# Optimization experiments

Measured on AMD Instinct MI355X. Metric: run time of the kernel, lower is better.

The kernel has to match this reference:

```python
import jax, jax.numpy as jnp
import numpy as np

H = 12          # num heads
D = 768         # hidden size
DH = D // H     # size per head
FF = 3072       # intermediate size
EPS = 1e-11


def gelu(x):
    # tanh approximation, matching the TF source exactly
    c = np.sqrt(2.0 / np.pi).astype(np.float32)
    return x * 0.5 * (1.0 + jnp.tanh(c * (x + 0.044715 * jnp.power(x, 3))))


def layer_norm(x, gamma, beta):
    mean = jnp.mean(x, axis=-1, keepdims=True)
    var = jnp.mean(jnp.square(x - mean), axis=-1, keepdims=True)
    return (x - mean) * jax.lax.rsqrt(var + EPS) * gamma + beta


def setup_inputs() -> dict:
    key = jax.random.key(0)
    ks = jax.random.split(key, 12)
    B, S = 16, 512
    std = 0.02
    inp = {
        "x": jax.random.normal(ks[0], (B, S, D), jnp.float32),
        "mask": jnp.ones((B, S), dtype=bool),
        "Wq": jax.random.normal(ks[1], (D, D), jnp.float32) * std,
        "bq": jnp.zeros((D,), jnp.float32),
        "Wk": jax.random.normal(ks[2], (D, D), jnp.float32) * std,
        "bk": jnp.zeros((D,), jnp.float32),
        "Wv": jax.random.normal(ks[3], (D, D), jnp.float32) * std,
        "bv": jnp.zeros((D,), jnp.float32),
        "Wo": jax.random.normal(ks[4], (D, D), jnp.float32) * std,
        "bo": jnp.zeros((D,), jnp.float32),
        "g1": jnp.ones((D,), jnp.float32),
        "b1": jnp.zeros((D,), jnp.float32),
        "Wi": jax.random.normal(ks[5], (D, FF), jnp.float32) * std,
        "bi": jnp.zeros((FF,), jnp.float32),
        "Wo2": jax.random.normal(ks[6], (FF, D), jnp.float32) * std,
        "bo2": jnp.zeros((D,), jnp.float32),
        "g2": jnp.ones((D,), jnp.float32),
        "b2": jnp.zeros((D,), jnp.float32),
    }
    return inp


def reference(x, mask, Wq, bq, Wk, bk, Wv, bv, Wo, bo, g1, b1, Wi, bi, Wo2, bo2, g2, b2):
    B, S, _ = x.shape
    # QKV projections
    q = (x @ Wq + bq).reshape(B, S, H, DH)
    k = (x @ Wk + bk).reshape(B, S, H, DH)
    v = (x @ Wv + bv).reshape(B, S, H, DH)
    # scaled dot-product attention scores [B, H, S, S]
    scores = jnp.einsum("bqhd,bkhd->bhqk", q, k) / np.sqrt(DH).astype(np.float32)
    # key-side mask, applied as score * m + (1 - m) * -100 (per original source)
    m = mask[:, None, None, :].astype(jnp.float32)
    scores = scores * m + (1.0 - m) * (-100.0)
    probs = jax.nn.softmax(scores, axis=-1)
    attn = jnp.einsum("bhqk,bkhd->bqhd", probs, v).reshape(B, S, D)
    # tf.boolean_mask with all-True mask -> flatten batch and seq dims
    attn = attn.reshape(B * S, D)
    x_flat = x.reshape(B * S, D)
    # attention output projection + residual + LN
    attn_out = layer_norm(attn @ Wo + bo + x_flat, g1, b1)
    # FFN: gelu dense then output dense + residual + LN
    inter = gelu(attn_out @ Wi + bi)
    out = layer_norm(inter @ Wo2 + bo2 + attn_out, g2, b2)
    return out
```

## Files before the change

kernel.cpp:

```cpp
#include <hip/hip_runtime.h>


#define DEV __device__ __forceinline__

typedef unsigned short u16;
typedef unsigned int   u32;
typedef __bf16 bf16x8 __attribute__((ext_vector_type(8)));
typedef float  f32x4  __attribute__((ext_vector_type(4)));
typedef unsigned short u16x8 __attribute__((ext_vector_type(8)));
typedef unsigned short u16x4 __attribute__((ext_vector_type(4)));

DEV u16 f2bf(float f) {
    u32 u = __builtin_bit_cast(u32, f);
    u += 0x7fffu + ((u >> 16) & 1u);
    return (u16)(u >> 16);
}

DEV float gelu_f(float x) {
    float u = 0.7978845608028654f * (x + 0.044715f * x * x * x);
    float e = __expf(2.f * u);
    return 0.5f * x * (2.f - 2.f / (e + 1.f));
}

DEV void gload16(const void* gsrc, void* ldst) {
    __builtin_amdgcn_global_load_lds(
        (__attribute__((address_space(1))) void*)(void*)(const_cast<void*>(gsrc)),
        (__attribute__((address_space(3))) void*)ldst, 16, 0, 0);
}

DEV f32x4 MFMA(bf16x8 a, bf16x8 b, f32x4 c) {
    return __builtin_amdgcn_mfma_f32_16x16x32_bf16(a, b, c, 0, 0, 0);
}

__global__ __launch_bounds__(256) void cvt_bf16(const float* __restrict__ in,
                                                u16* __restrict__ out, int n) {
    int i = (blockIdx.x * 256 + threadIdx.x) * 4;
    if (i >= n) return;
    f32x4 v = *(const f32x4*)(in + i);
    u16x4 o;
    o.x = f2bf(v.x); o.y = f2bf(v.y); o.z = f2bf(v.z); o.w = f2bf(v.w);
    *(u16x4*)(out + i) = o;
}

__global__ __launch_bounds__(256) void transpose_cvt(const float* __restrict__ in,
                                                     u16* __restrict__ out,
                                                     int R, int C) {
    __shared__ float tile[32][33];
    int tx = threadIdx.x & 31, ty = threadIdx.x >> 5;
    int r0 = blockIdx.y * 32, c0 = blockIdx.x * 32;
#pragma unroll
    for (int i = 0; i < 4; i++)
        tile[ty + i * 8][tx] = in[(size_t)(r0 + ty + i * 8) * C + c0 + tx];
    __syncthreads();
#pragma unroll
    for (int i = 0; i < 4; i++)
        out[(size_t)(c0 + ty + i * 8) * R + r0 + tx] = f2bf(tile[tx][ty + i * 8]);
}

__global__ void concat_bias(const float* __restrict__ bq, const float* __restrict__ bk,
                            const float* __restrict__ bv, float* __restrict__ o) {
    int i = blockIdx.x * 256 + threadIdx.x;
    if (i < 2304) o[i] = (i < 768) ? bq[i] : (i < 1536 ? bk[i - 768] : bv[i - 1536]);
}

template <int EPI>
DEV void gemm_hi_body(const u16* __restrict__ A, const u16* __restrict__ BT,
                      const float* __restrict__ bias, void* __restrict__ Cout,
                      int N, int K, int ntn) {
    __shared__ __align__(16) char smem[32768];
    const int t = threadIdx.x, lane = t & 63, wid = t >> 6;
    const int nwg = gridDim.x, bid = blockIdx.x;
    const int swzb = ((nwg & 7) == 0) ? ((bid & 7) * (nwg >> 3) + (bid >> 3)) : bid;
    const int tm = swzb / ntn, tn = swzb % ntn;
    const int wm = wid >> 1, wn = wid & 1;

    f32x4 acc[4][4];
#pragma unroll
    for (int i = 0; i < 4; i++)
#pragma unroll
        for (int j = 0; j < 4; j++) acc[i][j] = f32x4{0.f, 0.f, 0.f, 0.f};

    const int NT = K >> 5;
    const u16* Ab = A + (size_t)tm * 128 * K;
    const u16* Bb = BT + (size_t)tn * 128 * K;

    int sr[2], sc[2];
#pragma unroll
    for (int j = 0; j < 2; j++) {
        int X = t * 16 + j * 4096;
        int Y = X ^ (((X >> 7) & 7) << 4);
        sr[j] = Y >> 6;
        sc[j] = (Y & 63) >> 1;
    }
    const u16* pA0 = Ab + (size_t)sr[0] * K + sc[0];
    const u16* pA1 = Ab + (size_t)sr[1] * K + sc[1];
    const u16* pB0 = Bb + (size_t)sr[0] * K + sc[0];
    const u16* pB1 = Bb + (size_t)sr[1] * K + sc[1];
    const int d0 = wid * 1024, d1 = wid * 1024 + 4096;

    const int g16 = (lane >> 4) << 4;
    const int rA = wm * 64 + (lane & 15);
    const int rB = wn * 64 + (lane & 15);
    const int aoff = (rA * 64 + g16) ^ (((rA >> 1) & 7) << 4);
    const int boff = 8192 + ((rB * 64 + g16) ^ (((rB >> 1) & 7) << 4));

#define STG(KT, BUF)                                                  \
    {                                                                 \
        char* s_ = smem + (BUF) * 16384;                              \
        gload16(pA0 + (KT), s_ + d0);                                 \
        gload16(pA1 + (KT), s_ + d1);                                 \
        gload16(pB0 + (KT), s_ + 8192 + d0);                          \
        gload16(pB1 + (KT), s_ + 8192 + d1);                          \
    }

    STG(0, 0);
    __syncthreads();

    for (int kt = 0; kt < NT; ++kt) {
        if (kt + 1 < NT) STG((kt + 1) << 5, (kt & 1) ^ 1);
        const char* buf = smem + (kt & 1) * 16384;
        bf16x8 af[4], bfr[4];
#pragma unroll
        for (int mi = 0; mi < 4; mi++) af[mi] = *(const bf16x8*)(buf + aoff + mi * 1024);
#pragma unroll
        for (int ni = 0; ni < 4; ni++) bfr[ni] = *(const bf16x8*)(buf + boff + ni * 1024);
        __builtin_amdgcn_s_setprio(1);
#pragma unroll
        for (int mi = 0; mi < 4; mi++)
#pragma unroll
            for (int ni = 0; ni < 4; ni++)
                acc[mi][ni] = MFMA(af[mi], bfr[ni], acc[mi][ni]);
        __builtin_amdgcn_s_setprio(0);
        __syncthreads();
    }
#undef STG

    const int r0 = tm * 128 + wm * 64, c0 = tn * 128 + wn * 64;
    float bcol[4];
#pragma unroll
    for (int ni = 0; ni < 4; ni++) bcol[ni] = bias[c0 + ni * 16 + (lane & 15)];
#pragma unroll
    for (int mi = 0; mi < 4; mi++) {
#pragma unroll
        for (int r = 0; r < 4; r++) {
            int gr = r0 + mi * 16 + ((lane >> 4) << 2) + r;
#pragma unroll
            for (int ni = 0; ni < 4; ni++) {
                int gc = c0 + ni * 16 + (lane & 15);
                float v = acc[mi][ni][r] + bcol[ni];
                if constexpr (EPI == 2) v = gelu_f(v);
                if constexpr (EPI == 1)
                    ((float*)Cout)[(size_t)gr * N + gc] = v;
                else
                    ((u16*)Cout)[(size_t)gr * N + gc] = f2bf(v);
            }
        }
    }
}

__global__ __launch_bounds__(256, 4) void gemm_qkv(const u16* __restrict__ A,
                                                   const u16* __restrict__ BT,
                                                   const float* __restrict__ bias,
                                                   void* __restrict__ Cout,
                                                   int N, int K, int ntn) {
    gemm_hi_body<0>(A, BT, bias, Cout, N, K, ntn);
}
__global__ __launch_bounds__(256, 4) void gemm_wo(const u16* __restrict__ A,
                                                  const u16* __restrict__ BT,
                                                  const float* __restrict__ bias,
                                                  void* __restrict__ Cout,
                                                  int N, int K, int ntn) {
    gemm_hi_body<1>(A, BT, bias, Cout, N, K, ntn);
}
__global__ __launch_bounds__(256, 4) void gemm_ffn1(const u16* __restrict__ A,
                                                    const u16* __restrict__ BT,
                                                    const float* __restrict__ bias,
                                                    void* __restrict__ Cout,
                                                    int N, int K, int ntn) {
    gemm_hi_body<2>(A, BT, bias, Cout, N, K, ntn);
}
__global__ __launch_bounds__(256, 4) void gemm_ffn2(const u16* __restrict__ A,
                                                    const u16* __restrict__ BT,
                                                    const float* __restrict__ bias,
                                                    void* __restrict__ Cout,
                                                    int N, int K, int ntn) {
    gemm_hi_body<1>(A, BT, bias, Cout, N, K, ntn);
}

__global__ __launch_bounds__(256) void attn_kernel(const u16* __restrict__ QKV,
                                                   u16* __restrict__ attnb) {
    __shared__ __align__(16) char sm[24576];
    char* Ks = sm;
    char* Vt = sm + 8192;
    const int t = threadIdx.x, lane = t & 63, wid = t >> 6;
    const int qt = blockIdx.x, bh = blockIdx.y;
    const int b = bh / 12, h = bh % 12;
    const size_t base = (size_t)b * 512 * 2304;
    char* Pw = sm + 16384 + wid * 2048;

    bf16x8 aq[2];
    {
        int qrow = qt * 64 + wid * 16 + (lane & 15);
        const u16* qp = QKV + base + (size_t)qrow * 2304 + h * 64 + ((lane >> 4) << 3);
        aq[0] = *(const bf16x8*)qp;
        aq[1] = *(const bf16x8*)(qp + 32);
    }
    f32x4 oacc[4];
#pragma unroll
    for (int g = 0; g < 4; g++) oacc[g] = f32x4{0.f, 0.f, 0.f, 0.f};
    float mrun[4] = {-1e30f, -1e30f, -1e30f, -1e30f};
    float lrun[4] = {0.f, 0.f, 0.f, 0.f};

    for (int kt = 0; kt < 8; ++kt) {
        __syncthreads();
#pragma unroll
        for (int i = 0; i < 2; i++) {
            int cw = wid * 2 + i;
            int o = cw * 1024 + lane * 16;
            int row = o >> 7;
            int cb = (o & 127) ^ ((row & 7) << 4);
            gload16(QKV + base + (size_t)(kt * 64 + row) * 2304 + 768 + h * 64 + (cb >> 1),
                    Ks + cw * 1024);
        }
        {
            int key = t & 63, dh0 = wid * 16;
            const u16* vp = QKV + base + (size_t)(kt * 64 + key) * 2304 + 1536 + h * 64 + dh0;
            u16x8 v0 = *(const u16x8*)vp;
            u16x8 v1 = *(const u16x8*)(vp + 8);
#pragma unroll
            for (int j = 0; j < 8; j++) {
                int dh = dh0 + j;
                *(u16*)(Vt + dh * 128 + ((key * 2) ^ ((dh & 7) << 4))) = v0[j];
            }
#pragma unroll
            for (int j = 0; j < 8; j++) {
                int dh = dh0 + 8 + j;
                *(u16*)(Vt + dh * 128 + ((key * 2) ^ ((dh & 7) << 4))) = v1[j];
            }
        }
        __syncthreads();

        f32x4 sacc[4];
#pragma unroll
        for (int ni = 0; ni < 4; ni++) sacc[ni] = f32x4{0.f, 0.f, 0.f, 0.f};
#pragma unroll
        for (int ni = 0; ni < 4; ni++) {
            int row = ni * 16 + (lane & 15);
#pragma unroll
            for (int ks = 0; ks < 2; ks++) {
                int cb = (ks * 64 + ((lane >> 4) << 4)) ^ ((row & 7) << 4);
                bf16x8 bk = *(const bf16x8*)(Ks + row * 128 + cb);
                sacc[ni] = MFMA(aq[ks], bk, sacc[ni]);
            }
        }
#pragma unroll
        for (int ni = 0; ni < 4; ni++)
#pragma unroll
            for (int r = 0; r < 4; r++) sacc[ni][r] *= 0.125f;

#pragma unroll
        for (int r = 0; r < 4; r++) {
            float pm = fmaxf(fmaxf(sacc[0][r], sacc[1][r]), fmaxf(sacc[2][r], sacc[3][r]));
            pm = fmaxf(pm, __shfl_xor(pm, 1));
            pm = fmaxf(pm, __shfl_xor(pm, 2));
            pm = fmaxf(pm, __shfl_xor(pm, 4));
            pm = fmaxf(pm, __shfl_xor(pm, 8));
            float mnew = fmaxf(mrun[r], pm);
            float sf = __expf(mrun[r] - mnew);
            mrun[r] = mnew;
            lrun[r] *= sf;
#pragma unroll
            for (int g = 0; g < 4; g++) oacc[g][r] *= sf;
            int prow = ((lane >> 4) << 2) + r;
            float ps = 0.f;
#pragma unroll
            for (int ni = 0; ni < 4; ni++) {
                float p = __expf(sacc[ni][r] - mnew);
                ps += p;
                int col = ni * 16 + (lane & 15);
                *(u16*)(Pw + prow * 128 + ((col * 2) ^ ((prow & 7) << 4))) = f2bf(p);
            }
            ps += __shfl_xor(ps, 1);
            ps += __shfl_xor(ps, 2);
            ps += __shfl_xor(ps, 4);
            ps += __shfl_xor(ps, 8);
            lrun[r] += ps;
        }
        __syncthreads();

#pragma unroll
        for (int ks = 0; ks < 2; ks++) {
            int prow = lane & 15;
            int pcb = (ks * 64 + ((lane >> 4) << 4)) ^ ((prow & 7) << 4);
            bf16x8 ap = *(const bf16x8*)(Pw + prow * 128 + pcb);
#pragma unroll
            for (int g = 0; g < 4; g++) {
                int vrow = g * 16 + (lane & 15);
                int vcb = (ks * 64 + ((lane >> 4) << 4)) ^ ((vrow & 7) << 4);
                bf16x8 bv = *(const bf16x8*)(Vt + vrow * 128 + vcb);
                oacc[g] = MFMA(ap, bv, oacc[g]);
            }
        }
    }

#pragma unroll
    for (int g = 0; g < 4; g++)
#pragma unroll
        for (int r = 0; r < 4; r++) {
            int qrow = qt * 64 + wid * 16 + ((lane >> 4) << 2) + r;
            float o = oacc[g][r] / lrun[r];
            attnb[(size_t)(b * 512 + qrow) * 768 + h * 64 + g * 16 + (lane & 15)] = f2bf(o);
        }
}

__global__ __launch_bounds__(256) void ln_kernel(const float* __restrict__ Y,
                                                 const float* __restrict__ res,
                                                 const float* __restrict__ g,
                                                 const float* __restrict__ bta,
                                                 float* __restrict__ outf,
                                                 u16* __restrict__ outb) {
    int row = blockIdx.x, t = threadIdx.x, lane = t & 63, wid = t >> 6;
    const float* y = Y + (size_t)row * 768;
    const float* rr = res + (size_t)row * 768;
    float v[3];
#pragma unroll
    for (int i = 0; i < 3; i++) v[i] = y[t + i * 256] + rr[t + i * 256];

    float s = v[0] + v[1] + v[2];
#pragma unroll
    for (int o = 32; o; o >>= 1) s += __shfl_xor(s, o);
    __shared__ float sm[4];
    __shared__ float bc[2];
    if (lane == 0) sm[wid] = s;
    __syncthreads();
    if (t == 0) bc[0] = (sm[0] + sm[1] + sm[2] + sm[3]) * (1.f / 768.f);
    __syncthreads();
    float mean = bc[0];

    float q = 0.f;
#pragma unroll
    for (int i = 0; i < 3; i++) { float d = v[i] - mean; q += d * d; }
#pragma unroll
    for (int o = 32; o; o >>= 1) q += __shfl_xor(q, o);
    if (lane == 0) sm[wid] = q;
    __syncthreads();
    if (t == 0) bc[1] = rsqrtf((sm[0] + sm[1] + sm[2] + sm[3]) * (1.f / 768.f) + 1e-11f);
    __syncthreads();
    float rs = bc[1];
#pragma unroll
    for (int i = 0; i < 3; i++) {
        int c = t + i * 256;
        float o = (v[i] - mean) * rs * g[c] + bta[c];
        outf[(size_t)row * 768 + c] = o;
        if (outb) outb[(size_t)row * 768 + c] = f2bf(o);
    }
}

extern "C" void kernel_launch(void* const* d_in, const int* in_sizes, int n_in,
                              void* d_out, int out_size, void* d_ws, size_t ws_size,
                              hipStream_t stream) {
    const float* x   = (const float*)d_in[0];
    const float* Wq  = (const float*)d_in[2];
    const float* bq  = (const float*)d_in[3];
    const float* Wk  = (const float*)d_in[4];
    const float* bk  = (const float*)d_in[5];
    const float* Wv  = (const float*)d_in[6];
    const float* bv  = (const float*)d_in[7];
    const float* Wo  = (const float*)d_in[8];
    const float* bo  = (const float*)d_in[9];
    const float* g1  = (const float*)d_in[10];
    const float* b1  = (const float*)d_in[11];
    const float* Wi  = (const float*)d_in[12];
    const float* bi  = (const float*)d_in[13];
    const float* Wo2 = (const float*)d_in[14];
    const float* bo2 = (const float*)d_in[15];
    const float* g2  = (const float*)d_in[16];
    const float* b2  = (const float*)d_in[17];

    char* w = (char*)d_ws;
    size_t off = 0;
    auto alloc = [&](size_t n) { size_t o = off; off += (n + 255) & ~(size_t)255; return o; };
    size_t oXb    = alloc((size_t)8192 * 768 * 2);
    size_t oWqkvT = alloc((size_t)2304 * 768 * 2);
    size_t oWoT   = alloc((size_t)768 * 768 * 2);
    size_t oWiT   = alloc((size_t)3072 * 768 * 2);
    size_t oWo2T  = alloc((size_t)768 * 3072 * 2);
    size_t oBqkv  = alloc((size_t)2304 * 4);
    size_t oR0    = alloc((size_t)8192 * 3072 * 2);
    size_t oY     = alloc((size_t)8192 * 768 * 4);
    size_t oAof   = alloc((size_t)8192 * 768 * 4);
    size_t oAob   = alloc((size_t)8192 * 768 * 2);
    (void)ws_size; (void)in_sizes; (void)n_in; (void)out_size;

    u16*   Xb    = (u16*)(w + oXb);
    u16*   WqkvT = (u16*)(w + oWqkvT);
    u16*   WoT   = (u16*)(w + oWoT);
    u16*   WiT   = (u16*)(w + oWiT);
    u16*   Wo2T  = (u16*)(w + oWo2T);
    float* bqkv  = (float*)(w + oBqkv);
    u16*   QKV   = (u16*)(w + oR0);
    u16*   attnb = (u16*)(w + oR0 + (size_t)8192 * 2304 * 2);
    u16*   inter = (u16*)(w + oR0);
    float* Y     = (float*)(w + oY);
    float* aof   = (float*)(w + oAof);
    u16*   aob   = (u16*)(w + oAob);

    cvt_bf16<<<6144, 256, 0, stream>>>(x, Xb, 8192 * 768);
    transpose_cvt<<<dim3(24, 24), 256, 0, stream>>>(Wq, WqkvT, 768, 768);
    transpose_cvt<<<dim3(24, 24), 256, 0, stream>>>(Wk, WqkvT + 768 * 768, 768, 768);
    transpose_cvt<<<dim3(24, 24), 256, 0, stream>>>(Wv, WqkvT + 2 * 768 * 768, 768, 768);
    transpose_cvt<<<dim3(24, 24), 256, 0, stream>>>(Wo, WoT, 768, 768);
    transpose_cvt<<<dim3(96, 24), 256, 0, stream>>>(Wi, WiT, 768, 3072);
    transpose_cvt<<<dim3(24, 96), 256, 0, stream>>>(Wo2, Wo2T, 3072, 768);
    concat_bias<<<9, 256, 0, stream>>>(bq, bk, bv, bqkv);

    gemm_qkv<<<1152, 256, 0, stream>>>(Xb, WqkvT, bqkv, QKV, 2304, 768, 18);
    attn_kernel<<<dim3(8, 192), 256, 0, stream>>>(QKV, attnb);
    gemm_wo<<<384, 256, 0, stream>>>(attnb, WoT, bo, Y, 768, 768, 6);
    ln_kernel<<<8192, 256, 0, stream>>>(Y, x, g1, b1, aof, aob);
    gemm_ffn1<<<1536, 256, 0, stream>>>(aob, WiT, bi, inter, 3072, 768, 24);
    gemm_ffn2<<<384, 256, 0, stream>>>(inter, Wo2T, bo2, Y, 768, 3072, 6);
    ln_kernel<<<8192, 256, 0, stream>>>(Y, aof, g2, b2, (float*)d_out, nullptr);
}
```

Measured before the change: 281.1 us.

## Use 256x256-tile 8-wave pipelined GEMM for QKV and FFN1 projections

Adds a new GEMM kernel with 512 threads and a 256x256 output tile. It double-buffers 128 KB of LDS and interleaves the next chunk's global loads with MFMA phases, using barriers and s_setprio. The QKV and FFN1 projections move to this kernel, with fewer, larger workgroups, to raise data reuse per tile and overlap loads with compute. In exchange, LDS and register use rise sharply, limiting occupancy. The QKV grid of 288 blocks may also underfill the CUs or leave tail imbalance.

```diff
diff --git a/kernel.cpp b/kernel.cpp
--- a/kernel.cpp
+++ b/kernel.cpp
@@ -61,6 +61,169 @@
                             const float* __restrict__ bv, float* __restrict__ o) {
     int i = blockIdx.x * 256 + threadIdx.x;
     if (i < 2304) o[i] = (i < 768) ? bq[i] : (i < 1536 ? bk[i - 768] : bv[i - 1536]);
+}
+
+template <int EPI>
+DEV void gemm8p_body(const u16* __restrict__ A, const u16* __restrict__ BT,
+                     const float* __restrict__ bias, void* __restrict__ Cout,
+                     int N, int K, int ntn) {
+    __shared__ __align__(16) char smem[131072];
+    const int t = threadIdx.x, lane = t & 63, wid = t >> 6;
+    const int nwg = gridDim.x, bid = blockIdx.x;
+    const int swzb = ((nwg & 7) == 0) ? ((bid & 7) * (nwg >> 3) + (bid >> 3)) : bid;
+    const int tm = swzb / ntn, tn = swzb % ntn;
+    const int wm = wid >> 2, wn = wid & 3;
+
+    f32x4 acc[8][4];
+#pragma unroll
+    for (int m = 0; m < 8; m++)
+#pragma unroll
+        for (int n = 0; n < 4; n++) acc[m][n] = f32x4{0.f, 0.f, 0.f, 0.f};
+
+    const int NC = K >> 6;
+    const u16* Abp = A + (size_t)tm * 256 * K;
+    const u16* Bbp = BT + (size_t)tn * 256 * K;
+
+    int sr[2], sc[2];
+#pragma unroll
+    for (int j = 0; j < 2; j++) {
+        int X = t * 16 + j * 8192;
+        int Y = X ^ (((X >> 7) & 7) << 4);
+        sr[j] = Y >> 7;
+        sc[j] = (Y & 127) >> 1;
+    }
+    const u16* pA0 = Abp + (size_t)sr[0] * K + sc[0];
+    const u16* pA1 = Abp + (size_t)sr[1] * K + sc[1];
+    const u16* pB0 = Bbp + (size_t)sr[0] * K + sc[0];
+    const u16* pB1 = Bbp + (size_t)sr[1] * K + sc[1];
+    const int dst0 = wid * 1024, dst1 = wid * 1024 + 8192;
+
+    const int l15 = lane & 15, g16 = (lane >> 4) << 4, sw = (lane & 7) << 4;
+    const int aHB = wm * 16384;
+    const int bHB = 32768 + (wn >> 1) * 16384 + (wn & 1) * 8192;
+    const int rb = l15 * 128;
+    const int cb0 = g16 ^ sw, cb1 = (64 + g16) ^ sw;
+
+#define STG_A(C, H) { char* d_ = smem + ((C) & 1) * 65536 + (H) * 16384;      \
+    gload16(pA0 + (size_t)(H) * 128 * K + (size_t)(C) * 64, d_ + dst0);       \
+    gload16(pA1 + (size_t)(H) * 128 * K + (size_t)(C) * 64, d_ + dst1); }
+#define STG_B(C, H) { char* d_ = smem + ((C) & 1) * 65536 + 32768 + (H) * 16384; \
+    gload16(pB0 + (size_t)(H) * 128 * K + (size_t)(C) * 64, d_ + dst0);       \
+    gload16(pB1 + (size_t)(H) * 128 * K + (size_t)(C) * 64, d_ + dst1); }
+#define BAR  __builtin_amdgcn_s_barrier(); asm volatile("" ::: "memory");
+
+    STG_A(0, 0) STG_A(0, 1) STG_B(0, 0) STG_B(0, 1) STG_A(1, 0) STG_A(1, 1)
+    asm volatile("s_waitcnt vmcnt(4)" ::: "memory");
+    BAR
+
+    for (int c = 0; c < NC; ++c) {
+        const char* db = smem + (c & 1) * 65536;
+        bf16x8 Alo[4][2], Ahi[4][2], Bf[4][2];
+#pragma unroll
+        for (int mi = 0; mi < 4; mi++) {
+            Alo[mi][0] = *(const bf16x8*)(db + aHB + rb + mi * 2048 + cb0);
+            Alo[mi][1] = *(const bf16x8*)(db + aHB + rb + mi * 2048 + cb1);
+        }
+#pragma unroll
+        for (int ni = 0; ni < 4; ni++) {
+            Bf[ni][0] = *(const bf16x8*)(db + bHB + rb + ni * 2048 + cb0);
+            Bf[ni][1] = *(const bf16x8*)(db + bHB + rb + ni * 2048 + cb1);
+        }
+        if (c + 1 < NC) STG_B(c + 1, 0)
+        BAR
+        asm volatile("s_waitcnt lgkmcnt(0)" ::: "memory");
+        __builtin_amdgcn_s_setprio(1);
+#pragma unroll
+        for (int mi = 0; mi < 4; mi++)
+#pragma unroll
+            for (int ni = 0; ni < 2; ni++)
+#pragma unroll
+                for (int ks = 0; ks < 2; ks++)
+                    acc[mi][ni] = MFMA(Alo[mi][ks], Bf[ni][ks], acc[mi][ni]);
+        __builtin_amdgcn_s_setprio(0);
+        BAR
+#pragma unroll
+        for (int mi = 0; mi < 4; mi++) {
+            Ahi[mi][0] = *(const bf16x8*)(db + aHB + 8192 + rb + mi * 2048 + cb0);
+            Ahi[mi][1] = *(const bf16x8*)(db + aHB + 8192 + rb + mi * 2048 + cb1);
+        }
+        if (c + 1 < NC) STG_B(c + 1, 1)
+        BAR
+        asm volatile("s_waitcnt lgkmcnt(0)" ::: "memory");
+        __builtin_amdgcn_s_setprio(1);
+#pragma unroll
+        for (int mi = 0; mi < 4; mi++)
+#pragma unroll
+            for (int ni = 2; ni < 4; ni++)
+#pragma unroll
+                for (int ks = 0; ks < 2; ks++)
+                    acc[mi][ni] = MFMA(Alo[mi][ks], Bf[ni][ks], acc[mi][ni]);
+        __builtin_amdgcn_s_setprio(0);
+        BAR
+        if (c + 2 < NC) STG_A(c + 2, 0)
+        BAR
+        __builtin_amdgcn_s_setprio(1);
+#pragma unroll
+        for (int mi = 0; mi < 4; mi++)
+#pragma unroll
+            for (int ni = 0; ni < 2; ni++)
+#pragma unroll
+                for (int ks = 0; ks < 2; ks++)
+                    acc[4 + mi][ni] = MFMA(Ahi[mi][ks], Bf[ni][ks], acc[4 + mi][ni]);
+        __builtin_amdgcn_s_setprio(0);
+        BAR
+        if (c + 2 < NC) STG_A(c + 2, 1)
+        BAR
+        __builtin_amdgcn_s_setprio(1);
+#pragma unroll
+        for (int mi = 0; mi < 4; mi++)
+#pragma unroll
+            for (int ni = 2; ni < 4; ni++)
+#pragma unroll
+                for (int ks = 0; ks < 2; ks++)
+                    acc[4 + mi][ni] = MFMA(Ahi[mi][ks], Bf[ni][ks], acc[4 + mi][ni]);
+        __builtin_amdgcn_s_setprio(0);
+        if (c + 2 < NC) asm volatile("s_waitcnt vmcnt(4)" ::: "memory");
+        else            asm volatile("s_waitcnt vmcnt(0)" ::: "memory");
+        BAR
+    }
+#undef STG_A
+#undef STG_B
+#undef BAR
+
+    const int r0 = tm * 256 + wm * 128, c0 = tn * 256 + wn * 64;
+    float cb4[4];
+#pragma unroll
+    for (int ni = 0; ni < 4; ni++) cb4[ni] = bias[c0 + ni * 16 + l15];
+#pragma unroll
+    for (int m = 0; m < 8; m++) {
+#pragma unroll
+        for (int r = 0; r < 4; r++) {
+            int gr = r0 + m * 16 + ((lane >> 4) << 2) + r;
+#pragma unroll
+            for (int ni = 0; ni < 4; ni++) {
+                int gc = c0 + ni * 16 + l15;
+                float v = acc[m][ni][r] + cb4[ni];
+                if constexpr (EPI == 2) v = gelu_f(v);
+                ((u16*)Cout)[(size_t)gr * N + gc] = f2bf(v);
+            }
+        }
+    }
+}
+
+__global__ __launch_bounds__(512, 2) void g8_qkv(const u16* __restrict__ A,
+                                                 const u16* __restrict__ BT,
+                                                 const float* __restrict__ bias,
+                                                 void* __restrict__ Cout,
+                                                 int N, int K, int ntn) {
+    gemm8p_body<0>(A, BT, bias, Cout, N, K, ntn);
+}
+__global__ __launch_bounds__(512, 2) void g8_ffn1(const u16* __restrict__ A,
+                                                  const u16* __restrict__ BT,
+                                                  const float* __restrict__ bias,
+                                                  void* __restrict__ Cout,
+                                                  int N, int K, int ntn) {
+    gemm8p_body<2>(A, BT, bias, Cout, N, K, ntn);
 }
 
 template <int EPI>
@@ -158,26 +321,12 @@
     }
 }
 
-__global__ __launch_bounds__(256, 4) void gemm_qkv(const u16* __restrict__ A,
-                                                   const u16* __restrict__ BT,
-                                                   const float* __restrict__ bias,
-                                                   void* __restrict__ Cout,
-                                                   int N, int K, int ntn) {
-    gemm_hi_body<0>(A, BT, bias, Cout, N, K, ntn);
-}
 __global__ __launch_bounds__(256, 4) void gemm_wo(const u16* __restrict__ A,
                                                   const u16* __restrict__ BT,
                                                   const float* __restrict__ bias,
                                                   void* __restrict__ Cout,
                                                   int N, int K, int ntn) {
     gemm_hi_body<1>(A, BT, bias, Cout, N, K, ntn);
-}
-__global__ __launch_bounds__(256, 4) void gemm_ffn1(const u16* __restrict__ A,
-                                                    const u16* __restrict__ BT,
-                                                    const float* __restrict__ bias,
-                                                    void* __restrict__ Cout,
-                                                    int N, int K, int ntn) {
-    gemm_hi_body<2>(A, BT, bias, Cout, N, K, ntn);
 }
 __global__ __launch_bounds__(256, 4) void gemm_ffn2(const u16* __restrict__ A,
                                                     const u16* __restrict__ BT,
@@ -414,11 +563,11 @@
     transpose_cvt<<<dim3(24, 96), 256, 0, stream>>>(Wo2, Wo2T, 3072, 768);
     concat_bias<<<9, 256, 0, stream>>>(bq, bk, bv, bqkv);
 
-    gemm_qkv<<<1152, 256, 0, stream>>>(Xb, WqkvT, bqkv, QKV, 2304, 768, 18);
+    g8_qkv<<<288, 512, 0, stream>>>(Xb, WqkvT, bqkv, QKV, 2304, 768, 9);
     attn_kernel<<<dim3(8, 192), 256, 0, stream>>>(QKV, attnb);
     gemm_wo<<<384, 256, 0, stream>>>(attnb, WoT, bo, Y, 768, 768, 6);
     ln_kernel<<<8192, 256, 0, stream>>>(Y, x, g1, b1, aof, aob);
-    gemm_ffn1<<<1536, 256, 0, stream>>>(aob, WiT, bi, inter, 3072, 768, 24);
+    g8_ffn1<<<384, 512, 0, stream>>>(aob, WiT, bi, inter, 3072, 768, 12);
     gemm_ffn2<<<384, 256, 0, stream>>>(inter, Wo2T, bo2, Y, 768, 3072, 6);
     ln_kernel<<<8192, 256, 0, stream>>>(Y, aof, g2, b2, (float*)d_out, nullptr);
 }
```

New measurement: 299.6 us. 6.6% more time.
